# Optimization experiments

Measured on AMD Instinct MI355X. Metric: run time of the kernel, lower is better.

The kernel has to match this reference:

```python
import jax, jax.numpy as jnp
import numpy as np

B, T, D, H = 16, 64, 256, 1536  # batch, num_seq (trg_len), input_dim, hid_dim


def setup_inputs() -> dict:
    key = jax.random.key(0)
    ks = jax.random.split(key, 6)
    def w(k, shape, fan):
        return jax.random.normal(k, shape, jnp.float32) / np.sqrt(fan).astype(np.float32)
    return {
        "batch": jax.random.normal(ks[0], (B, T, D), jnp.float32),
        # PyTorch LSTM params, gate order (i, f, g, o), layer 0 and layer 1
        "W_ih0": w(ks[1], (4 * H, D), H),
        "W_hh0": w(ks[2], (4 * H, H), H),
        "b_ih0": jnp.zeros((4 * H,), jnp.float32),
        "b_hh0": jnp.zeros((4 * H,), jnp.float32),
        "W_ih1": w(ks[3], (4 * H, H), H),
        "W_hh1": w(ks[4], (4 * H, H), H),
        "b_ih1": jnp.zeros((4 * H,), jnp.float32),
        "b_hh1": jnp.zeros((4 * H,), jnp.float32),
    }


def _lstm_cell(pre, c):
    # pre: [4H] pre-activation gates in PyTorch order i, f, g, o
    i, f, g, o = jnp.split(pre, 4, axis=-1)
    c_new = jax.nn.sigmoid(f) * c + jax.nn.sigmoid(i) * jnp.tanh(g)
    h_new = jax.nn.sigmoid(o) * jnp.tanh(c_new)
    return h_new, c_new


def reference(batch, W_ih0, W_hh0, b_ih0, b_hh0, W_ih1, W_hh1, b_ih1, b_hh1):
    hdim = W_hh0.shape[1]
    dt = batch.dtype
    # The original loop runs the unbatched 2-layer LSTM over batch[:, ei, :]
    # (length-B sequence) for ei = 1..T-1, carrying state => one scan over a
    # flattened sequence of length (T-1)*B, ordered ei-major, b-minor.
    seq = batch[:, 1:, :].transpose(1, 0, 2).reshape(-1, batch.shape[2])  # [(T-1)*B, D]
    # Precompute layer-0 input projection as one GEMM (dropout=0.3 is between
    # layers in train mode only; reference is eval mode, so no dropout).
    x_pre0 = seq @ W_ih0.T + (b_ih0 + b_hh0)  # [(T-1)*B, 4H]
    b1 = b_ih1 + b_hh1

    def step(carry, xp0):
        h, c = carry  # each [2, H] (num_layers, hid_dim), unbatched
        h0, c0 = _lstm_cell(xp0 + h[0] @ W_hh0.T, c[0])
        h1, c1 = _lstm_cell(h0 @ W_ih1.T + h[1] @ W_hh1.T + b1, c[1])
        return (jnp.stack([h0, h1]), jnp.stack([c0, c1])), None

    init = (jnp.zeros((2, hdim), dt), jnp.zeros((2, hdim), dt))
    (h_final, c_final), _ = jax.lax.scan(step, init, x_pre0)
    return h_final, c_final  # each [2, H], matching (encoder_hidden, encoder_cell)
```

## Files before the change

kernel.cpp:

```cpp
#include <hip/hip_runtime.h>
#include <cstdint>

#define HDIM   1536
#define DIN    256
#define NSTEP  1008
#define NWG    256
#define TPB    512
#define UPW    6
#define XN     256

#define C_H0      0
#define C_H1      1024
#define WS_FLAG_W 4096

typedef uint32_t u32x4 __attribute__((ext_vector_type(4)));

__device__ __forceinline__ float bflo(uint32_t p){ union{uint32_t u; float f;} v; v.u = p << 16; return v.f; }
__device__ __forceinline__ float bfhi(uint32_t p){ union{uint32_t u; float f;} v; v.u = p & 0xffff0000u; return v.f; }
__device__ __forceinline__ float bf2f(uint16_t b){ union{uint32_t u; float f;} v; v.u = ((uint32_t)b) << 16; return v.f; }
__device__ __forceinline__ uint16_t f2bf(float f){
    union{float f; uint32_t u;} v; v.f = f;
    uint32_t r = v.u + 0x7fffu + ((v.u >> 16) & 1u);
    return (uint16_t)(r >> 16);
}
__device__ __forceinline__ uint32_t packbf(float lo, float hi){
    return (uint32_t)f2bf(lo) | ((uint32_t)f2bf(hi) << 16);
}
__device__ __forceinline__ float tanh_fast(float x){
    return 1.f - 2.f/(__expf(2.f*x) + 1.f);
}

#if __has_builtin(__builtin_amdgcn_fdot2_f32_bf16)
typedef __bf16 bf16x2 __attribute__((ext_vector_type(2)));
__device__ __forceinline__ float dot2bf(uint32_t a, uint32_t b, float c){
    return __builtin_amdgcn_fdot2_f32_bf16(__builtin_bit_cast(bf16x2, a),
                                           __builtin_bit_cast(bf16x2, b), c, false);
}
#else
__device__ __forceinline__ float dot2bf(uint32_t a, uint32_t b, float c){
    c = fmaf(bflo(a), bflo(b), c);
    c = fmaf(bfhi(a), bfhi(b), c);
    return c;
}
#endif

__device__ __forceinline__ u32x4 poll16(const uint64_t* p){
    u32x4 r;
    asm volatile("global_load_dwordx4 %0, %1, off sc0 sc1\n\t"
                 "s_waitcnt vmcnt(0)"
                 : "=v"(r) : "v"(p) : "memory");
    return r;
}

__device__ __forceinline__ float wave_sum(float x){
    #pragma unroll
    for (int o = 1; o < 64; o <<= 1) x += __shfl_xor(x, o, 64);
    return x;
}

__global__ void init_ws(const uint32_t* __restrict__ w, uint32_t* __restrict__ ws){
    uint64_t* ws64 = (uint64_t*)ws;
    const int i = blockIdx.x * blockDim.x + threadIdx.x;
    if (i < 512){
        ws64[C_H0 + 512 + i] = 0ull;
        ws64[C_H1 + i]       = 0ull;
        ws64[C_H1 + 512 + i] = ((uint64_t)1 << 48);
    }
    if (blockIdx.x == 0 && threadIdx.x < 64){
        const int t = threadIdx.x;
        int cnt = 0;
        #pragma unroll
        for (int j = 0; j < 4; ++j){
            const uint32_t v = w[t*4 + j];
            const uint32_t e = (v >> 7) & 0xFFu;
            if (e == 0u || (e >= 0x70u && e <= 0x7Cu)) cnt++;
        }
        #pragma unroll
        for (int o = 1; o < 64; o <<= 1) cnt += __shfl_xor(cnt, o, 64);
        if (t == 0)
            ws[WS_FLAG_W] = (cnt < 128) ? 1u : 0u;
    }
}

__global__ __launch_bounds__(TPB, 2)
void lstm_seq_kernel(const void* __restrict__ batch_,
                     const void* __restrict__ Wih0_,
                     const void* __restrict__ Whh0_,
                     const void* __restrict__ bih0_,
                     const void* __restrict__ bhh0_,
                     const void* __restrict__ Wih1_,
                     const void* __restrict__ Whh1_,
                     const void* __restrict__ bih1_,
                     const void* __restrict__ bhh1_,
                     void* __restrict__ out_,
                     uint32_t* __restrict__ ws)
{
    __shared__ uint32_t lds_w[8*3*8*64];
    __shared__ uint32_t lds_h[1536];
    __shared__ float    lds_pre[48];
    __shared__ float    lds_b[48];
    __shared__ float    lds_c[12];
    __shared__ float    lds_hout[12];

    const int g   = blockIdx.x;
    const int tid = threadIdx.x;
    const int w   = tid >> 6;
    const int l   = tid & 63;

    const uint32_t fp32in = __hip_atomic_load(&ws[WS_FLAG_W],
                             __ATOMIC_RELAXED, __HIP_MEMORY_SCOPE_AGENT);
    uint64_t* ws64 = (uint64_t*)ws;

    if (tid < 24){
        const int uu = tid >> 2, gate = tid & 3;
        const int grow = gate*HDIM + g*UPW + uu;
        if (fp32in){
            lds_b[tid]      = ((const float*)bih0_)[grow] + ((const float*)bhh0_)[grow];
            lds_b[24 + tid] = ((const float*)bih1_)[grow] + ((const float*)bhh1_)[grow];
        } else {
            lds_b[tid]      = bf2f(((const uint16_t*)bih0_)[grow]) + bf2f(((const uint16_t*)bhh0_)[grow]);
            lds_b[24 + tid] = bf2f(((const uint16_t*)bih1_)[grow]) + bf2f(((const uint16_t*)bhh1_)[grow]);
        }
    }
    if (tid < 12){ lds_c[tid] = 0.f; lds_hout[tid] = 0.f; }

    uint32_t w0[3][14];
    uint32_t w1r[3][16];

    if (fp32in){
        const float2* Wih0f = (const float2*)Wih0_;
        const float2* Whh0f = (const float2*)Whh0_;
        const float2* Wih1f = (const float2*)Wih1_;
        const float2* Whh1f = (const float2*)Whh1_;
        #pragma unroll
        for (int j = 0; j < 3; ++j){
            const int rr = w*3 + j;
            const int grow = (rr & 3)*HDIM + g*UPW + (rr >> 2);
            float2 t;
            t = Wih0f[grow*(DIN/2) + l];        w0[j][0] = packbf(t.x, t.y);
            t = Wih0f[grow*(DIN/2) + 64 + l];   w0[j][1] = packbf(t.x, t.y);
            #pragma unroll
            for (int c = 2; c < 14; ++c){
                t = Whh0f[grow*(HDIM/2) + (c-2)*64 + l]; w0[j][c] = packbf(t.x, t.y);
            }
            #pragma unroll
            for (int c = 0; c < 8; ++c){
                t = Wih1f[grow*(HDIM/2) + c*64 + l];
                lds_w[((w*3 + j)*8 + c)*64 + l] = packbf(t.x, t.y);
            }
            #pragma unroll
            for (int c = 8; c < 12; ++c){
                t = Wih1f[grow*(HDIM/2) + c*64 + l]; w1r[j][c-8] = packbf(t.x, t.y);
            }
            #pragma unroll
            for (int c = 12; c < 24; ++c){
                t = Whh1f[grow*(HDIM/2) + (c-12)*64 + l]; w1r[j][c-8] = packbf(t.x, t.y);
            }
        }
    } else {
        const uint32_t* Wih0p = (const uint32_t*)Wih0_;
        const uint32_t* Whh0p = (const uint32_t*)Whh0_;
        const uint32_t* Wih1p = (const uint32_t*)Wih1_;
        const uint32_t* Whh1p = (const uint32_t*)Whh1_;
        #pragma unroll
        for (int j = 0; j < 3; ++j){
            const int rr = w*3 + j;
            const int grow = (rr & 3)*HDIM + g*UPW + (rr >> 2);
            w0[j][0] = Wih0p[grow*(DIN/2) + l];
            w0[j][1] = Wih0p[grow*(DIN/2) + 64 + l];
            #pragma unroll
            for (int c = 2; c < 14; ++c)
                w0[j][c] = Whh0p[grow*(HDIM/2) + (c-2)*64 + l];
            #pragma unroll
            for (int c = 0; c < 8; ++c)
                lds_w[((w*3 + j)*8 + c)*64 + l] = Wih1p[grow*(HDIM/2) + c*64 + l];
            #pragma unroll
            for (int c = 8; c < 12; ++c)
                w1r[j][c-8] = Wih1p[grow*(HDIM/2) + c*64 + l];
            #pragma unroll
            for (int c = 12; c < 24; ++c)
                w1r[j][c-8] = Whh1p[grow*(HDIM/2) + (c-12)*64 + l];
        }
    }

    const int players = tid >> 8;
    const int pidx    = tid & 255;

    for (int n = 0; n <= NSTEP; ++n){
        uint32_t xp0, xp1;
        {
            const int nn = (n < NSTEP) ? n : 0;
            const int xbase = ((nn & 15)*64 + (nn >> 4) + 1) * XN;
            if (fp32in){
                const float2* bp = (const float2*)((const float*)batch_ + xbase);
                const float2 t0 = bp[l];
                const float2 t1 = bp[64 + l];
                xp0 = packbf(t0.x, t0.y); xp1 = packbf(t1.x, t1.y);
            } else {
                const uint32_t* bp = (const uint32_t*)batch_ + (xbase >> 1);
                xp0 = bp[l]; xp1 = bp[64 + l];
            }
        }

        u32x4 r;
        {
            const uint64_t* ap = ws64
                + (players ? (C_H1 + (n & 1)*512) : (C_H0 + ((n+1) & 1)*512))
                + 2*pidx;
            const uint32_t want = (uint32_t)n & 0xFFFFu;
            r = poll16(ap);
            while ((r.y >> 16) != want || (r.w >> 16) != want){
                __builtin_amdgcn_s_sleep(2);
                r = poll16(ap);
            }
        }
        {
            const int base = players*768 + 3*pidx;
            lds_h[base]     = r.x;
            lds_h[base + 1] = (r.y & 0xFFFFu) | (r.z << 16);
            lds_h[base + 2] = (r.z >> 16)     | (r.w << 16);
        }
        __syncthreads();

        uint32_t h0p[12], h1p[12];
        #pragma unroll
        for (int k = 0; k < 12; ++k) h0p[k] = lds_h[k*64 + l];
        #pragma unroll
        for (int k = 0; k < 12; ++k) h1p[k] = lds_h[768 + k*64 + l];

        float acc0[3], acc1[3];
        #pragma unroll
        for (int j = 0; j < 3; ++j){
            float a = dot2bf(w0[j][0], xp0, 0.f);
            a = dot2bf(w0[j][1], xp1, a);
            #pragma unroll
            for (int k = 0; k < 12; ++k)
                a = dot2bf(w0[j][k+2], h0p[k], a);
            acc0[j] = a;
        }
        #pragma unroll
        for (int j = 0; j < 3; ++j){
            float a = 0.f;
            #pragma unroll
            for (int k = 0; k < 8; ++k)
                a = dot2bf(lds_w[((w*3 + j)*8 + k)*64 + l], h0p[k], a);
            #pragma unroll
            for (int k = 8; k < 12; ++k)
                a = dot2bf(w1r[j][k-8], h0p[k], a);
            #pragma unroll
            for (int k = 0; k < 12; ++k)
                a = dot2bf(w1r[j][k+4], h1p[k], a);
            acc1[j] = a;
        }
        #pragma unroll
        for (int j = 0; j < 3; ++j){
            const float r0 = wave_sum(acc0[j]);
            const float r1 = wave_sum(acc1[j]);
            if (l == 0){
                lds_pre[w*3 + j]      = r0;
                lds_pre[24 + w*3 + j] = r1;
            }
        }
        __syncthreads();

        if (w == 0){
            float hpub = 0.f;
            if (l < 12){
                const int layer = l / 6, uu = l % 6;
                const bool active = (layer == 0) ? (n < NSTEP) : (n >= 1);
                if (active){
                    const float* pre = &lds_pre[layer*24 + uu*4];
                    const float* bb  = &lds_b[layer*24 + uu*4];
                    const float gi = pre[0] + bb[0];
                    const float gf = pre[1] + bb[1];
                    const float gg = pre[2] + bb[2];
                    const float go = pre[3] + bb[3];
                    const float si = 1.f/(1.f + __expf(-gi));
                    const float sf = 1.f/(1.f + __expf(-gf));
                    const float so = 1.f/(1.f + __expf(-go));
                    const float cn = sf*lds_c[l] + si*tanh_fast(gg);
                    const float hn = so * tanh_fast(cn);
                    lds_c[l] = cn;
                    lds_hout[l] = hn;
                    hpub = hn;
                }
            }
            const float s0 = __shfl(hpub, (3*l)     & 63, 64);
            const float s1 = __shfl(hpub, (3*l + 1) & 63, 64);
            const float s2 = __shfl(hpub, (3*l + 2) & 63, 64);
            if (l < 4 && n < NSTEP){
                const bool isL1 = (l >= 2);
                if (!isL1 || n >= 1){
                    const uint64_t tag = (uint64_t)((uint32_t)(n + 1) & 0xFFFFu);
                    const uint64_t pk = (uint64_t)f2bf(s0)
                                      | ((uint64_t)f2bf(s1) << 16)
                                      | ((uint64_t)f2bf(s2) << 32)
                                      | (tag << 48);
                    uint64_t* dst = isL1
                        ? (ws64 + C_H1 + ((n+1) & 1)*512 + 2*g + (l - 2))
                        : (ws64 + C_H0 + (n & 1)*512 + 2*g + l);
                    __hip_atomic_store(dst, pk, __ATOMIC_RELAXED, __HIP_MEMORY_SCOPE_AGENT);
                }
            }
        }
    }

    if (tid < 12){
        const int layer = tid / 6, uu = tid % 6;
        const int oi = layer*HDIM + g*UPW + uu;
        if (fp32in){
            ((float*)out_)[oi]        = lds_hout[tid];
            ((float*)out_)[3072 + oi] = lds_c[tid];
        } else {
            ((uint16_t*)out_)[oi]        = f2bf(lds_hout[tid]);
            ((uint16_t*)out_)[3072 + oi] = f2bf(lds_c[tid]);
        }
    }
}

extern "C" void kernel_launch(void* const* d_in, const int* in_sizes, int n_in,
                              void* d_out, int out_size, void* d_ws, size_t ws_size,
                              hipStream_t stream)
{
    (void)in_sizes; (void)n_in; (void)out_size; (void)ws_size;
    const void* batch = d_in[0];
    const void* Wih0  = d_in[1];
    const void* Whh0  = d_in[2];
    const void* bih0  = d_in[3];
    const void* bhh0  = d_in[4];
    const void* Wih1  = d_in[5];
    const void* Whh1  = d_in[6];
    const void* bih1  = d_in[7];
    const void* bhh1  = d_in[8];
    void* out = d_out;
    uint32_t* ws = (uint32_t*)d_ws;

    hipLaunchKernelGGL(init_ws, dim3(2), dim3(256), 0, stream,
                       (const uint32_t*)Whh0, ws);

    void* args[] = { &batch, &Wih0, &Whh0, &bih0, &bhh0,
                     &Wih1, &Whh1, &bih1, &bhh1, &out, &ws };
    hipLaunchCooperativeKernel((const void*)lstm_seq_kernel,
                               dim3(NWG), dim3(TPB), args, 0, stream);
}
```

Baseline: 3.644 ms.

## Replicate hidden-state exchange buffers across workgroups to spread polling traffic

Each workgroup now publishes its hidden-state fragments into eight replicated copies of the exchange buffer, and each workgroup polls only the replica chosen by its index. This aims to reduce contention when all 256 workgroups spin on the same cache lines during the per-step grid-wide handoff. Each step now does eight times as many atomic stores, and the workspace layout and init kernel grow to match. The poll sleep interval is also shortened.

```diff
diff --git a/kernel.cpp b/kernel.cpp
--- a/kernel.cpp
+++ b/kernel.cpp
@@ -8,10 +8,12 @@
 #define TPB    512
 #define UPW    6
 #define XN     256
+#define NREP   8
 
 #define C_H0      0
 #define C_H1      1024
-#define WS_FLAG_W 4096
+#define REP_STRIDE 2048
+#define WS_FLAG_W 32768
 
 typedef uint32_t u32x4 __attribute__((ext_vector_type(4)));
 
@@ -61,10 +63,12 @@
 __global__ void init_ws(const uint32_t* __restrict__ w, uint32_t* __restrict__ ws){
     uint64_t* ws64 = (uint64_t*)ws;
     const int i = blockIdx.x * blockDim.x + threadIdx.x;
-    if (i < 512){
-        ws64[C_H0 + 512 + i] = 0ull;
-        ws64[C_H1 + i]       = 0ull;
-        ws64[C_H1 + 512 + i] = ((uint64_t)1 << 48);
+    if (i < NREP*512){
+        const int rep = i >> 9, j = i & 511;
+        uint64_t* base = ws64 + rep*REP_STRIDE;
+        base[C_H0 + 512 + j] = 0ull;
+        base[C_H1 + j]       = 0ull;
+        base[C_H1 + 512 + j] = ((uint64_t)1 << 48);
     }
     if (blockIdx.x == 0 && threadIdx.x < 64){
         const int t = threadIdx.x;
@@ -185,6 +189,7 @@
 
     const int players = tid >> 8;
     const int pidx    = tid & 255;
+    uint64_t* myrep   = ws64 + (g & (NREP-1))*REP_STRIDE;
 
     for (int n = 0; n <= NSTEP; ++n){
         uint32_t xp0, xp1;
@@ -204,13 +209,13 @@
 
         u32x4 r;
         {
-            const uint64_t* ap = ws64
+            const uint64_t* ap = myrep
                 + (players ? (C_H1 + (n & 1)*512) : (C_H0 + ((n+1) & 1)*512))
                 + 2*pidx;
             const uint32_t want = (uint32_t)n & 0xFFFFu;
             r = poll16(ap);
             while ((r.y >> 16) != want || (r.w >> 16) != want){
-                __builtin_amdgcn_s_sleep(2);
+                __builtin_amdgcn_s_sleep(1);
                 r = poll16(ap);
             }
         }
@@ -285,20 +290,22 @@
                     hpub = hn;
                 }
             }
-            const float s0 = __shfl(hpub, (3*l)     & 63, 64);
-            const float s1 = __shfl(hpub, (3*l + 1) & 63, 64);
-            const float s2 = __shfl(hpub, (3*l + 2) & 63, 64);
-            if (l < 4 && n < NSTEP){
-                const bool isL1 = (l >= 2);
+            const int slot = l & 3;
+            const int b3 = 3*slot;
+            const float s0 = __shfl(hpub, b3,     64);
+            const float s1 = __shfl(hpub, b3 + 1, 64);
+            const float s2 = __shfl(hpub, b3 + 2, 64);
+            if (l < 4*NREP && n < NSTEP){
+                const bool isL1 = (slot >= 2);
                 if (!isL1 || n >= 1){
                     const uint64_t tag = (uint64_t)((uint32_t)(n + 1) & 0xFFFFu);
                     const uint64_t pk = (uint64_t)f2bf(s0)
                                       | ((uint64_t)f2bf(s1) << 16)
                                       | ((uint64_t)f2bf(s2) << 32)
                                       | (tag << 48);
-                    uint64_t* dst = isL1
-                        ? (ws64 + C_H1 + ((n+1) & 1)*512 + 2*g + (l - 2))
-                        : (ws64 + C_H0 + (n & 1)*512 + 2*g + l);
+                    uint64_t* dst = ws64 + (l >> 2)*REP_STRIDE
+                        + (isL1 ? (C_H1 + ((n+1) & 1)*512 + 2*g + (slot - 2))
+                                : (C_H0 + (n & 1)*512 + 2*g + slot));
                     __hip_atomic_store(dst, pk, __ATOMIC_RELAXED, __HIP_MEMORY_SCOPE_AGENT);
                 }
             }
@@ -335,7 +342,7 @@
     void* out = d_out;
     uint32_t* ws = (uint32_t*)d_ws;
 
-    hipLaunchKernelGGL(init_ws, dim3(2), dim3(256), 0, stream,
+    hipLaunchKernelGGL(init_ws, dim3((NREP*512 + 255)/256), dim3(256), 0, stream,
                        (const uint32_t*)Whh0, ws);
 
     void* args[] = { &batch, &Wih0, &Whh0, &bih0, &bhh0,
```

Measured after the change: 3.506 ms. -3.8%, faster.
